# Kernel tuning notes

Hardware: AMD Instinct MI355X
Metric: run time of the kernel (lower is better)

The kernel has to match this reference:

```python
import jax, jax.numpy as jnp
import numpy as np

S = 1024   # speakers_per_batch
U = 64     # utterances_per_speaker
D = 256    # embedding_size
EPS = 1e-5


def setup_inputs() -> dict:
    key = jax.random.key(0)
    k1, = jax.random.split(key, 1)
    return {
        "output_of_model": jax.random.normal(k1, (S * U, D), dtype=jnp.float32),
        "similarity_weight": jnp.array([10.0], dtype=jnp.float32),
        "similarity_bias": jnp.array([-5.0], dtype=jnp.float32),
        "speakers_per_batch": S,
        "utterances_per_speaker": U,
    }


def reference(output_of_model, similarity_weight, similarity_bias,
              speakers_per_batch, utterances_per_speaker):
    s, u = speakers_per_batch, utterances_per_speaker
    embeds = output_of_model.reshape(s, u, -1)                      # [S,U,D]

    # inclusive centroids (mean over utterances, L2-normalized with +eps)
    c_incl = jnp.mean(embeds, axis=1)                               # [S,D]
    c_incl = c_incl / (jnp.linalg.norm(c_incl, axis=-1, keepdims=True) + EPS)

    # exclusive centroids (leave-one-out mean, L2-normalized with +eps)
    c_excl = (jnp.sum(embeds, axis=1, keepdims=True) - embeds) / (u - 1)  # [S,U,D]
    c_excl = c_excl / (jnp.linalg.norm(c_excl, axis=-1, keepdims=True) + EPS)

    # normalized embeddings (original normalizes embeds inside the loop)
    e_n = embeds / (jnp.linalg.norm(embeds, axis=-1, keepdims=True) + EPS)

    # off-diagonal: cosine(embed[i,u], incl centroid[j]); diagonal: excl centroid
    sim_incl = jnp.einsum('sud,jd->suj', e_n, c_incl)               # [S,U,S]
    sim_excl = jnp.sum(e_n * c_excl, axis=-1)                       # [S,U]
    diag = jnp.eye(s, dtype=bool)[:, None, :]                       # [S,1,S]
    sim = jnp.where(diag, sim_excl[:, :, None], sim_incl)           # [S,U,S]

    sim = sim * similarity_weight + similarity_bias                 # scaled logits

    logits = sim.reshape(s * u, s)
    targets = jnp.repeat(jnp.arange(s), u)                          # ground truth
    logp = jax.nn.log_softmax(logits, axis=-1)
    loss = -jnp.mean(jnp.take_along_axis(logp, targets[:, None], axis=-1))
    return loss
```

## Files before the change

kernel.cpp:

```cpp
#include <hip/hip_runtime.h>

#define SPK 1024
#define UTT 64
#define DIM 256
#define EPSV 1e-5f
#define NROW (SPK * UTT)
#define NSL 8
#define LOG2E 1.44269504f

typedef __attribute__((ext_vector_type(4))) float f32x4;

#define EXP2(x) __builtin_amdgcn_exp2f(x)

__device__ __forceinline__ int pk_fp8(float a, float b, float c, float d) {
    int v = __builtin_amdgcn_cvt_pk_fp8_f32(a, b, 0, false);
    return  __builtin_amdgcn_cvt_pk_fp8_f32(c, d, v, true);
}

__global__ __launch_bounds__(256)
void k_prep(const float* __restrict__ x,
            unsigned char* __restrict__ cincl8,
            unsigned char* __restrict__ en8,
            float* __restrict__ texcl,
            const float* __restrict__ wp, const float* __restrict__ bp) {
    __shared__ float4 sc4[256];
    __shared__ float4 cs4[64];
    __shared__ float sccs;
    int s = blockIdx.x, tid = threadIdx.x;
    int dq = tid & 63, ug = tid >> 6;
    const float4* x4 = (const float4*)(x + (size_t)s * UTT * DIM);

    float4 p = {0.f, 0.f, 0.f, 0.f};
#pragma unroll
    for (int i = 0; i < 16; ++i) {
        float4 v = x4[(ug * 16 + i) * 64 + dq];
        p.x += v.x; p.y += v.y; p.z += v.z; p.w += v.w;
    }
    sc4[tid] = p;
    __syncthreads();
    if (tid < 64) {
        float4 a = sc4[dq], b2 = sc4[64 + dq], c = sc4[128 + dq], d = sc4[192 + dq];
        float4 cs = {a.x + b2.x + c.x + d.x, a.y + b2.y + c.y + d.y,
                     a.z + b2.z + c.z + d.z, a.w + b2.w + c.w + d.w};
        cs4[dq] = cs;
        float s2 = cs.x * cs.x + cs.y * cs.y + cs.z * cs.z + cs.w * cs.w;
#pragma unroll
        for (int o = 1; o < 64; o <<= 1) s2 += __shfl_xor(s2, o);
        if (tid == 0) sccs = s2;
        float inv = 16.f / (sqrtf(s2) + UTT * EPSV);
        ((int*)cincl8)[s * 64 + dq] =
            pk_fp8(cs.x * inv, cs.y * inv, cs.z * inv, cs.w * inv);
    }
    __syncthreads();
    float scc = sccs;
    float w = wp[0], b = bp[0];

    int row = tid >> 2, sub = tid & 3;
    const float4* xr = x4 + row * 64;
    float4 xv[16];
    float sx = 0.f, sc = 0.f;
#pragma unroll
    for (int i = 0; i < 16; ++i) {
        float4 v = xr[i * 4 + sub];
        float4 cv = cs4[i * 4 + sub];
        xv[i] = v;
        sx += v.x * v.x + v.y * v.y + v.z * v.z + v.w * v.w;
        sc += v.x * cv.x + v.y * cv.y + v.z * cv.z + v.w * cv.w;
    }
    sx += __shfl_xor(sx, 1); sx += __shfl_xor(sx, 2);
    sc += __shfl_xor(sc, 1); sc += __shfl_xor(sc, 2);
    float nx = sqrtf(sx);
    float inv = 16.f / (nx + EPSV);
    int* er = (int*)(en8 + (size_t)(s * UTT + row) * DIM);
#pragma unroll
    for (int i = 0; i < 16; ++i)
        er[i * 4 + sub] = pk_fp8(xv[i].x * inv, xv[i].y * inv,
                                 xv[i].z * inv, xv[i].w * inv);
    if (sub == 0) {
        float num = sc - sx;
        float e2 = fmaxf(scc - 2.f * sc + sx, 0.f);
        float sim = num / ((nx + EPSV) * (sqrtf(e2) + (UTT - 1) * EPSV));
        texcl[s * UTT + row] = fmaf(sim, w, b);
    }
}

__global__ __launch_bounds__(256, 3)
void k_main(const unsigned char* __restrict__ en8,
            const unsigned char* __restrict__ cincl8,
            float* __restrict__ partial,
            const float* __restrict__ wp, const float* __restrict__ bp) {
    __shared__ unsigned char Bs[64 * 512];
    int tid = threadIdx.x, wave = tid >> 6, lane = tid & 63;
    int quad = lane >> 4, lx = lane & 15;
    int bid = blockIdx.x;
    int xcd = bid & 7, j = bid >> 3;
    int cs = j & 7;
    int sg = xcd + 8 * (j >> 3);
    int sw = sg * 4 + wave;
    float w = wp[0], b = bp[0];
    float M  = fabsf(w) * 1.0625f + b;
    float wl = w * (LOG2E / 256.f);
    float bl = (b - M) * LOG2E;

#pragma unroll
    for (int nti = 0; nti < 2; ++nti) {
        int nt = wave * 2 + nti;
#pragma unroll
        for (int kp = 0; kp < 4; ++kp) {
            int kt = kp * 2 + (lane >> 5);
            int m = lane & 31, slx = m >> 1, h = m & 1;
            const unsigned char* g = cincl8 +
                (size_t)(cs * 128 + nt * 16 + slx) * DIM + kt * 32 + h * 16;
            __builtin_amdgcn_global_load_lds(
                (const __attribute__((address_space(1))) void*)g,
                (__attribute__((address_space(3))) void*)(Bs + (nt * 8 + kp * 2) * 512),
                16, 0, 0);
        }
    }

    const unsigned char* abase = en8 + (size_t)sw * UTT * DIM;
    long af[4][8];
#pragma unroll
    for (int mt = 0; mt < 4; ++mt)
#pragma unroll
        for (int kt = 0; kt < 8; ++kt)
            af[mt][kt] = *(const long*)(abase + (mt * 16 + lx) * DIM + kt * 32 + quad * 8);

    float l[16];
#pragma unroll
    for (int i = 0; i < 16; ++i) l[i] = 0.f;

    __syncthreads();

    int dnt = (sw >> 4) - cs * 8;
    int dlx = sw & 15;

    for (int nt = 0; nt < 8; ++nt) {
        long bf[8];
#pragma unroll
        for (int kt = 0; kt < 8; ++kt)
            bf[kt] = *(const long*)(Bs + (nt * 8 + kt) * 512 + lx * 32 + quad * 8);
        f32x4 aA[4] = {{0.f,0.f,0.f,0.f},{0.f,0.f,0.f,0.f},
                       {0.f,0.f,0.f,0.f},{0.f,0.f,0.f,0.f}};
        f32x4 aB[4] = {{0.f,0.f,0.f,0.f},{0.f,0.f,0.f,0.f},
                       {0.f,0.f,0.f,0.f},{0.f,0.f,0.f,0.f}};
#pragma unroll
        for (int kt = 0; kt < 4; ++kt) {
            aA[0] = __builtin_amdgcn_mfma_f32_16x16x32_fp8_fp8(af[0][kt], bf[kt], aA[0], 0, 0, 0);
            aA[1] = __builtin_amdgcn_mfma_f32_16x16x32_fp8_fp8(af[1][kt], bf[kt], aA[1], 0, 0, 0);
            aA[2] = __builtin_amdgcn_mfma_f32_16x16x32_fp8_fp8(af[2][kt], bf[kt], aA[2], 0, 0, 0);
            aA[3] = __builtin_amdgcn_mfma_f32_16x16x32_fp8_fp8(af[3][kt], bf[kt], aA[3], 0, 0, 0);
            aB[0] = __builtin_amdgcn_mfma_f32_16x16x32_fp8_fp8(af[0][kt+4], bf[kt+4], aB[0], 0, 0, 0);
            aB[1] = __builtin_amdgcn_mfma_f32_16x16x32_fp8_fp8(af[1][kt+4], bf[kt+4], aB[1], 0, 0, 0);
            aB[2] = __builtin_amdgcn_mfma_f32_16x16x32_fp8_fp8(af[2][kt+4], bf[kt+4], aB[2], 0, 0, 0);
            aB[3] = __builtin_amdgcn_mfma_f32_16x16x32_fp8_fp8(af[3][kt+4], bf[kt+4], aB[3], 0, 0, 0);
        }
#pragma unroll
        for (int mt = 0; mt < 4; ++mt)
#pragma unroll
            for (int r = 0; r < 4; ++r)
                l[mt * 4 + r] += EXP2(fmaf(aA[mt][r] + aB[mt][r], wl, bl));
        if (nt == dnt) {
#pragma unroll
            for (int mt = 0; mt < 4; ++mt)
#pragma unroll
                for (int r = 0; r < 4; ++r) {
                    float e = EXP2(fmaf(aA[mt][r] + aB[mt][r], wl, bl));
                    if (lx == dlx) l[mt * 4 + r] -= e;
                }
        }
    }

#pragma unroll
    for (int o = 1; o < 16; o <<= 1)
#pragma unroll
        for (int i = 0; i < 16; ++i) l[i] += __shfl_xor(l[i], o);
    if (lx == 0)
#pragma unroll
        for (int mt = 0; mt < 4; ++mt)
#pragma unroll
            for (int r = 0; r < 4; ++r)
                partial[(size_t)cs * NROW + (size_t)sw * UTT + mt * 16 + quad * 4 + r]
                    = l[mt * 4 + r];
}

__global__ __launch_bounds__(256)
void k_final(const float* __restrict__ partial, const float* __restrict__ texcl,
             const float* __restrict__ wp, const float* __restrict__ bp,
             float* __restrict__ out) {
    int row = blockIdx.x * 256 + threadIdx.x;
    float w = wp[0], b = bp[0];
    float M = fabsf(w) * 1.0625f + b;
    float t = 0.f;
#pragma unroll
    for (int sl = 0; sl < NSL; ++sl) t += partial[(size_t)sl * NROW + row];
    float tex = texcl[row];
    float c = (M + __logf(t + EXP2((tex - M) * LOG2E))) - tex;
#pragma unroll
    for (int o = 1; o < 64; o <<= 1) c += __shfl_xor(c, o);
    __shared__ float red[4];
    if ((threadIdx.x & 63) == 0) red[threadIdx.x >> 6] = c;
    __syncthreads();
    if (threadIdx.x == 0)
        atomicAdd(out, (red[0] + red[1] + red[2] + red[3]) * (1.f / NROW));
}

extern "C" void kernel_launch(void* const* d_in, const int* in_sizes, int n_in,
                              void* d_out, int out_size, void* d_ws, size_t ws_size,
                              hipStream_t stream) {
    const float* x  = (const float*)d_in[0];
    const float* wp = (const float*)d_in[1];
    const float* bp = (const float*)d_in[2];
    char* ws = (char*)d_ws;
    unsigned char* cincl8 = (unsigned char*)ws;
    float* texcl          = (float*)(ws + (1u << 19));
    float* partial        = (float*)(ws + (1u << 20));
    unsigned char* en8    = (unsigned char*)(ws + (4u << 20));
    float* out = (float*)d_out;

    hipMemsetAsync(d_out, 0, sizeof(float), stream);
    k_prep <<<SPK, 256, 0, stream>>>(x, cincl8, en8, texcl, wp, bp);
    k_main <<<(SPK / 4) * NSL, 256, 0, stream>>>(en8, cincl8, partial, wp, bp);
    k_final<<<NROW / 256, 256, 0, stream>>>(partial, texcl, wp, bp, out);
}
```

Baseline: 149.6 us.

## Permute fp8 K layout so MFMA fragments load as 16-byte vectors

The prep kernel now writes fp8 embeddings and centroids in a permuted K order (fragIdx), so each lane's two k-tile fragments are contiguous. The main kernel loads A from global and B from LDS with 128-bit loads instead of 64-bit ones, and the LDS staging layout is reorganised to match. This halves the number of load instructions and is meant to improve LDS access patterns. Since the dot product is invariant to a consistent K permutation, correctness depends on both operands using the same mapping.

```diff
diff --git a/kernel.cpp b/kernel.cpp
--- a/kernel.cpp
+++ b/kernel.cpp
@@ -9,12 +9,17 @@
 #define LOG2E 1.44269504f
 
 typedef __attribute__((ext_vector_type(4))) float f32x4;
+typedef __attribute__((ext_vector_type(2))) long long2v;
 
 #define EXP2(x) __builtin_amdgcn_exp2f(x)
 
 __device__ __forceinline__ int pk_fp8(float a, float b, float c, float d) {
     int v = __builtin_amdgcn_cvt_pk_fp8_f32(a, b, 0, false);
     return  __builtin_amdgcn_cvt_pk_fp8_f32(c, d, v, true);
+}
+
+__device__ __forceinline__ int fragIdx(int g) {
+    return ((g >> 4) * 4 + ((g & 7) >> 1)) * 4 + ((g >> 3) & 1) * 2 + (g & 1);
 }
 
 __global__ __launch_bounds__(256)
@@ -48,7 +53,7 @@
         for (int o = 1; o < 64; o <<= 1) s2 += __shfl_xor(s2, o);
         if (tid == 0) sccs = s2;
         float inv = 16.f / (sqrtf(s2) + UTT * EPSV);
-        ((int*)cincl8)[s * 64 + dq] =
+        ((int*)cincl8)[s * 64 + fragIdx(dq)] =
             pk_fp8(cs.x * inv, cs.y * inv, cs.z * inv, cs.w * inv);
     }
     __syncthreads();
@@ -74,8 +79,8 @@
     int* er = (int*)(en8 + (size_t)(s * UTT + row) * DIM);
 #pragma unroll
     for (int i = 0; i < 16; ++i)
-        er[i * 4 + sub] = pk_fp8(xv[i].x * inv, xv[i].y * inv,
-                                 xv[i].z * inv, xv[i].w * inv);
+        er[fragIdx(i * 4 + sub)] = pk_fp8(xv[i].x * inv, xv[i].y * inv,
+                                          xv[i].z * inv, xv[i].w * inv);
     if (sub == 0) {
         float num = sc - sx;
         float e2 = fmaxf(scc - 2.f * sc + sx, 0.f);
@@ -89,7 +94,7 @@
             const unsigned char* __restrict__ cincl8,
             float* __restrict__ partial,
             const float* __restrict__ wp, const float* __restrict__ bp) {
-    __shared__ unsigned char Bs[64 * 512];
+    __shared__ unsigned char Bs[32 * 1024];
     int tid = threadIdx.x, wave = tid >> 6, lane = tid & 63;
     int quad = lane >> 4, lx = lane & 15;
     int bid = blockIdx.x;
@@ -106,25 +111,23 @@
     for (int nti = 0; nti < 2; ++nti) {
         int nt = wave * 2 + nti;
 #pragma unroll
-        for (int kp = 0; kp < 4; ++kp) {
-            int kt = kp * 2 + (lane >> 5);
-            int m = lane & 31, slx = m >> 1, h = m & 1;
+        for (int r = 0; r < 4; ++r) {
             const unsigned char* g = cincl8 +
-                (size_t)(cs * 128 + nt * 16 + slx) * DIM + kt * 32 + h * 16;
+                (size_t)(cs * 128 + nt * 16 + lx) * DIM + (r * 4 + quad) * 16;
             __builtin_amdgcn_global_load_lds(
                 (const __attribute__((address_space(1))) void*)g,
-                (__attribute__((address_space(3))) void*)(Bs + (nt * 8 + kp * 2) * 512),
+                (__attribute__((address_space(3))) void*)(Bs + (nt * 4 + r) * 1024),
                 16, 0, 0);
         }
     }
 
     const unsigned char* abase = en8 + (size_t)sw * UTT * DIM;
-    long af[4][8];
+    long2v af2[4][4];
 #pragma unroll
     for (int mt = 0; mt < 4; ++mt)
 #pragma unroll
-        for (int kt = 0; kt < 8; ++kt)
-            af[mt][kt] = *(const long*)(abase + (mt * 16 + lx) * DIM + kt * 32 + quad * 8);
+        for (int r = 0; r < 4; ++r)
+            af2[mt][r] = *(const long2v*)(abase + (mt * 16 + lx) * DIM + (r * 4 + quad) * 16);
 
     float l[16];
 #pragma unroll
@@ -136,24 +139,26 @@
     int dlx = sw & 15;
 
     for (int nt = 0; nt < 8; ++nt) {
-        long bf[8];
-#pragma unroll
-        for (int kt = 0; kt < 8; ++kt)
-            bf[kt] = *(const long*)(Bs + (nt * 8 + kt) * 512 + lx * 32 + quad * 8);
+        long2v bf2[4];
+#pragma unroll
+        for (int r = 0; r < 4; ++r)
+            bf2[r] = *(const long2v*)(Bs + (nt * 4 + r) * 1024 + lane * 16);
         f32x4 aA[4] = {{0.f,0.f,0.f,0.f},{0.f,0.f,0.f,0.f},
                        {0.f,0.f,0.f,0.f},{0.f,0.f,0.f,0.f}};
         f32x4 aB[4] = {{0.f,0.f,0.f,0.f},{0.f,0.f,0.f,0.f},
                        {0.f,0.f,0.f,0.f},{0.f,0.f,0.f,0.f}};
 #pragma unroll
-        for (int kt = 0; kt < 4; ++kt) {
-            aA[0] = __builtin_amdgcn_mfma_f32_16x16x32_fp8_fp8(af[0][kt], bf[kt], aA[0], 0, 0, 0);
-            aA[1] = __builtin_amdgcn_mfma_f32_16x16x32_fp8_fp8(af[1][kt], bf[kt], aA[1], 0, 0, 0);
-            aA[2] = __builtin_amdgcn_mfma_f32_16x16x32_fp8_fp8(af[2][kt], bf[kt], aA[2], 0, 0, 0);
-            aA[3] = __builtin_amdgcn_mfma_f32_16x16x32_fp8_fp8(af[3][kt], bf[kt], aA[3], 0, 0, 0);
-            aB[0] = __builtin_amdgcn_mfma_f32_16x16x32_fp8_fp8(af[0][kt+4], bf[kt+4], aB[0], 0, 0, 0);
-            aB[1] = __builtin_amdgcn_mfma_f32_16x16x32_fp8_fp8(af[1][kt+4], bf[kt+4], aB[1], 0, 0, 0);
-            aB[2] = __builtin_amdgcn_mfma_f32_16x16x32_fp8_fp8(af[2][kt+4], bf[kt+4], aB[2], 0, 0, 0);
-            aB[3] = __builtin_amdgcn_mfma_f32_16x16x32_fp8_fp8(af[3][kt+4], bf[kt+4], aB[3], 0, 0, 0);
+        for (int r = 0; r < 2; ++r) {
+#pragma unroll
+            for (int mt = 0; mt < 4; ++mt) {
+                aA[mt] = __builtin_amdgcn_mfma_f32_16x16x32_fp8_fp8(af2[mt][r].x,   bf2[r].x,   aA[mt], 0, 0, 0);
+                aB[mt] = __builtin_amdgcn_mfma_f32_16x16x32_fp8_fp8(af2[mt][r+2].x, bf2[r+2].x, aB[mt], 0, 0, 0);
+            }
+#pragma unroll
+            for (int mt = 0; mt < 4; ++mt) {
+                aA[mt] = __builtin_amdgcn_mfma_f32_16x16x32_fp8_fp8(af2[mt][r].y,   bf2[r].y,   aA[mt], 0, 0, 0);
+                aB[mt] = __builtin_amdgcn_mfma_f32_16x16x32_fp8_fp8(af2[mt][r+2].y, bf2[r+2].y, aB[mt], 0, 0, 0);
+            }
         }
 #pragma unroll
         for (int mt = 0; mt < 4; ++mt)
```

Result: faster. 143.1 us (-4.3%).
